# Performance work log

Hardware: AMD Instinct MI355X
Metric: run time of the kernel (lower is better)

## Reference

```python
import jax, jax.numpy as jnp
import numpy as np

N_NODES = 50000
N_EDGES = 800000
D = 128


def setup_inputs() -> dict:
    key = jax.random.key(0)
    k1, k2, k3, k4 = jax.random.split(key, 4)
    feat = jax.random.normal(k1, (N_NODES, D), dtype=jnp.float32)
    W = jax.random.normal(k2, (D, D), dtype=jnp.float32) * (1.0 / np.sqrt(D))
    b = jnp.zeros((D,), dtype=jnp.float32)
    eps = jnp.zeros((1,), dtype=jnp.float32)
    src = jax.random.randint(k3, (N_EDGES,), 0, N_NODES, dtype=jnp.int64 if jax.config.jax_enable_x64 else jnp.int32)
    dst = jax.random.randint(k4, (N_EDGES,), 0, N_NODES, dtype=jnp.int64 if jax.config.jax_enable_x64 else jnp.int32)
    return {"feat": feat, "W": W, "b": b, "eps": eps, "src": src, "dst": dst}


def reference(feat, W, b, eps, src, dst):
    # message passing: m_e = feat[src_e]; neigh_i = sum_{e: dst_e = i} m_e
    msgs = feat[src]  # [E, D] gather
    neigh = jax.ops.segment_sum(msgs, dst, num_segments=N_NODES)  # [N, D]
    # eps-weighted residual: (1 + eps) * h_dst + neigh
    rst = (1.0 + eps) * feat + neigh  # eps is [1], broadcasts
    # apply_func: Dense(D)
    out = jnp.einsum('nd,de->ne', rst, W) + b
    return out
```

## Files before the change

kernel.cpp:

```cpp
#include <hip/hip_runtime.h>

#define D 128
#define CAP 32
#define OCAP 4096
#define TILE 16

typedef __attribute__((ext_vector_type(8))) short bf16x8;
typedef __attribute__((ext_vector_type(4))) float f32x4;

static __device__ inline short f2bf(float f) {
  union { float f; unsigned u; } v; v.f = f;
  unsigned r = v.u + 0x7FFF + ((v.u >> 16) & 1);
  return (short)(r >> 16);
}
static __device__ inline float bf_lo(unsigned u) {
  union { unsigned u; float f; } v; v.u = u << 16; return v.f;
}
static __device__ inline float bf_hi(unsigned u) {
  union { unsigned u; float f; } v; v.u = u & 0xFFFF0000u; return v.f;
}

static __device__ inline void wfrag_build_one(const float* __restrict__ W,
                                              uint4* __restrict__ wfrag, int t) {
  int c = t >> 8, h = (t >> 6) & 3, l = t & 63;
  int col = c * 16 + (l & 15);
  int k0 = h * 32 + (l >> 4) * 8;
  unsigned u[4];
  #pragma unroll
  for (int p = 0; p < 4; ++p) {
    unsigned lo = (unsigned short)f2bf(W[(k0 + 2 * p) * D + col]);
    unsigned hi = (unsigned short)f2bf(W[(k0 + 2 * p + 1) * D + col]);
    u[p] = lo | (hi << 16);
  }
  wfrag[t] = make_uint4(u[0], u[1], u[2], u[3]);
}

__global__ __launch_bounds__(256) void build_kernel(
    const int* __restrict__ src, const int* __restrict__ dst,
    int* __restrict__ cnt, int* __restrict__ ocount, unsigned* __restrict__ oflow,
    unsigned short* __restrict__ permfix,
    const float* __restrict__ W, uint4* __restrict__ wfrag,
    const float* __restrict__ feat, uint4* __restrict__ featbf,
    int E, int ND8) {
  int grp = blockIdx.x & 7;
  int e = (blockIdx.x >> 3) * 256 + threadIdx.x;
  if (e < E) {
    int d = dst[e];
    if (((d >> 5) & 7) == grp) {
      int s = src[e];
      int c = atomicAdd(&cnt[d], 1);
      if (c < CAP) {
        permfix[(size_t)d * CAP + c] = (unsigned short)s;
      } else {
        int o = atomicAdd(ocount, 1);
        if (o < OCAP) oflow[o] = ((unsigned)d << 16) | (unsigned)s;
      }
    }
  }
  int i = blockIdx.x * 256 + threadIdx.x;
  if (i < ND8) {
    float4 u = ((const float4*)feat)[2 * i];
    float4 v = ((const float4*)feat)[2 * i + 1];
    unsigned w0 = (unsigned short)f2bf(u.x) | ((unsigned)(unsigned short)f2bf(u.y) << 16);
    unsigned w1 = (unsigned short)f2bf(u.z) | ((unsigned)(unsigned short)f2bf(u.w) << 16);
    unsigned w2 = (unsigned short)f2bf(v.x) | ((unsigned)(unsigned short)f2bf(v.y) << 16);
    unsigned w3 = (unsigned short)f2bf(v.z) | ((unsigned)(unsigned short)f2bf(v.w) << 16);
    featbf[i] = make_uint4(w0, w1, w2, w3);
  }
  if (i < 2048) wfrag_build_one(W, wfrag, i);
}

static __device__ inline void gather8m(uint4 q, int jb, int deg, int nm1,
                                       const uint2* __restrict__ featbf, int lane,
                                       float4& acc) {
  unsigned wds[4] = {q.x, q.y, q.z, q.w};
  uint2 r[8];
  #pragma unroll
  for (int k = 0; k < 4; ++k) {
    int s0 = (int)(wds[k] & 0xFFFFu);
    int s1 = (int)(wds[k] >> 16);
    s0 = min(s0, nm1);
    s1 = min(s1, nm1);
    r[2 * k]     = featbf[(size_t)s0 * 32 + lane];
    r[2 * k + 1] = featbf[(size_t)s1 * 32 + lane];
  }
  #pragma unroll
  for (int k = 0; k < 8; ++k) {
    bool v = (jb + k) < deg;
    unsigned x = v ? r[k].x : 0u;
    unsigned y = v ? r[k].y : 0u;
    acc.x += bf_lo(x); acc.y += bf_hi(x);
    acc.z += bf_lo(y); acc.w += bf_hi(y);
  }
}

__global__ __launch_bounds__(128, 4) void fused_gather_gemm(
    const uint2* __restrict__ featbf, const float* __restrict__ eps,
    const float* __restrict__ bias, const int* __restrict__ cnt,
    const int* __restrict__ ocount, const unsigned* __restrict__ oflow,
    const unsigned short* __restrict__ permfix,
    const uint4* __restrict__ wfrag, float* __restrict__ out, int N) {
  __shared__ float xs[TILE][132];
  __shared__ float sbias[128];
  int tid = threadIdx.x;
  int base = blockIdx.x * TILE;
  sbias[tid] = bias[tid];
  float scale = 1.0f + eps[0];
  int nm1 = N - 1;

  int g = tid >> 5, lane = tid & 31;
  #pragma unroll
  for (int it = 0; it < TILE / 4; ++it) {
    int lr = it * 4 + g;
    int grow = base + lr;
    float4 acc = make_float4(0.f, 0.f, 0.f, 0.f);
    if (grow < N) {
      const uint4* pf4 = (const uint4*)(permfix + (size_t)grow * CAP);
      int deg = cnt[grow];
      deg = (deg < CAP) ? deg : CAP;
      uint2 a0 = featbf[(size_t)grow * 32 + lane];
      uint4 q0 = pf4[0];
      uint4 q1 = pf4[1];
      acc.x = scale * bf_lo(a0.x);
      acc.y = scale * bf_hi(a0.x);
      acc.z = scale * bf_lo(a0.y);
      acc.w = scale * bf_hi(a0.y);
      gather8m(q0, 0, deg, nm1, featbf, lane, acc);
      gather8m(q1, 8, deg, nm1, featbf, lane, acc);
      if (deg > 16) {
        uint4 q2 = pf4[2];
        gather8m(q2, 16, deg, nm1, featbf, lane, acc);
        if (deg > 24) {
          uint4 q3 = pf4[3];
          gather8m(q3, 24, deg, nm1, featbf, lane, acc);
        }
      }
    }
    *(float4*)&xs[lr][lane * 4] = acc;
  }
  __syncthreads();

  int novf = *ocount;
  novf = (novf < OCAP) ? novf : OCAP;
  if (novf > 0) {
    if (tid < 32) {
      for (int o = 0; o < novf; ++o) {
        unsigned e = oflow[o];
        int d = (int)(e >> 16);
        if ((d / TILE) == (int)blockIdx.x) {
          int s = (int)(e & 0xFFFF);
          uint2 a = featbf[(size_t)s * 32 + tid];
          int r = d % TILE;
          xs[r][tid * 4 + 0] += bf_lo(a.x);
          xs[r][tid * 4 + 1] += bf_hi(a.x);
          xs[r][tid * 4 + 2] += bf_lo(a.y);
          xs[r][tid * 4 + 3] += bf_hi(a.y);
        }
      }
    }
    __syncthreads();
  }

  int w = tid >> 6;
  int l = tid & 63;
  int rowg = l >> 4, rl = l & 15;
  int cb = w * 4;

  bf16x8 a[4];
  #pragma unroll
  for (int h = 0; h < 4; ++h) {
    const float* p = &xs[rl][h * 32 + rowg * 8];
    float4 u = *(const float4*)p;
    float4 v = *(const float4*)(p + 4);
    bf16x8 t;
    t[0] = f2bf(u.x); t[1] = f2bf(u.y); t[2] = f2bf(u.z); t[3] = f2bf(u.w);
    t[4] = f2bf(v.x); t[5] = f2bf(v.y); t[6] = f2bf(v.z); t[7] = f2bf(v.w);
    a[h] = t;
  }

  const bf16x8* wf = (const bf16x8*)wfrag;
  #pragma unroll
  for (int cl = 0; cl < 4; ++cl) {
    int c = cb + cl;
    float bb = sbias[c * 16 + rl];
    f32x4 acc = {bb, bb, bb, bb};
    #pragma unroll
    for (int h = 0; h < 4; ++h) {
      bf16x8 b = wf[(c * 4 + h) * 64 + l];
      acc = __builtin_amdgcn_mfma_f32_16x16x32_bf16(a[h], b, acc, 0, 0, 0);
    }
    #pragma unroll
    for (int r = 0; r < 4; ++r) {
      int row = base + rowg * 4 + r;
      if (row < N) out[(size_t)row * D + c * 16 + rl] = acc[r];
    }
  }
}

__global__ __launch_bounds__(256) void init_out_kernel(
    const float* __restrict__ feat, const float* __restrict__ eps,
    float* __restrict__ out, int n4) {
  int i = blockIdx.x * blockDim.x + threadIdx.x;
  if (i >= n4) return;
  float scale = 1.0f + eps[0];
  float4 v = ((const float4*)feat)[i];
  v.x *= scale; v.y *= scale; v.z *= scale; v.w *= scale;
  ((float4*)out)[i] = v;
}

__global__ __launch_bounds__(256) void scatter_add_kernel(
    const float* __restrict__ feat, const int* __restrict__ src,
    const int* __restrict__ dst, float* __restrict__ out, int E) {
  int gid = blockIdx.x * blockDim.x + threadIdx.x;
  int e = gid >> 5;
  int lane = gid & 31;
  if (e >= E) return;
  int s = src[e], d = dst[e];
  float4 v = ((const float4*)(feat + (size_t)s * D))[lane];
  float* o = out + (size_t)d * D + lane * 4;
  unsafeAtomicAdd(o + 0, v.x);
  unsafeAtomicAdd(o + 1, v.y);
  unsafeAtomicAdd(o + 2, v.z);
  unsafeAtomicAdd(o + 3, v.w);
}

#define ROWS 64
__global__ __launch_bounds__(256) void gemm_inplace_kernel(
    float* __restrict__ out, const float* __restrict__ Wm,
    const float* __restrict__ bias, int N) {
  __shared__ float Ws[D * D];
  __shared__ float xs[ROWS * D];
  int tid = threadIdx.x;
  int base = blockIdx.x * ROWS;
  #pragma unroll
  for (int it = 0; it < 16; ++it) {
    int idx = tid + 256 * it;
    ((float4*)Ws)[idx] = ((const float4*)Wm)[idx];
  }
  #pragma unroll
  for (int it = 0; it < 8; ++it) {
    int idx = tid + 256 * it;
    int row = idx >> 5, c4 = idx & 31;
    float4 v = make_float4(0.f, 0.f, 0.f, 0.f);
    if (base + row < N) v = ((const float4*)(out + (size_t)(base + row) * D))[c4];
    ((float4*)xs)[row * 32 + c4] = v;
  }
  __syncthreads();
  int tc = tid & 31, tr = tid >> 5;
  float acc[8][4];
  #pragma unroll
  for (int r = 0; r < 8; ++r)
    #pragma unroll
    for (int i = 0; i < 4; ++i) acc[r][i] = 0.f;
  for (int k0 = 0; k0 < D; k0 += 4) {
    float4 f[8];
    #pragma unroll
    for (int r = 0; r < 8; ++r) f[r] = *(const float4*)&xs[(tr * 8 + r) * D + k0];
    float w[4][4];
    #pragma unroll
    for (int u = 0; u < 4; ++u)
      #pragma unroll
      for (int i = 0; i < 4; ++i) w[u][i] = Ws[(k0 + u) * D + tc + 32 * i];
    #pragma unroll
    for (int r = 0; r < 8; ++r)
      #pragma unroll
      for (int i = 0; i < 4; ++i) {
        acc[r][i] += f[r].x * w[0][i];
        acc[r][i] += f[r].y * w[1][i];
        acc[r][i] += f[r].z * w[2][i];
        acc[r][i] += f[r].w * w[3][i];
      }
  }
  float bv[4];
  #pragma unroll
  for (int i = 0; i < 4; ++i) bv[i] = bias[tc + 32 * i];
  #pragma unroll
  for (int r = 0; r < 8; ++r) {
    int row = base + tr * 8 + r;
    if (row < N) {
      #pragma unroll
      for (int i = 0; i < 4; ++i)
        out[(size_t)row * D + tc + 32 * i] = acc[r][i] + bv[i];
    }
  }
}

extern "C" void kernel_launch(void* const* d_in, const int* in_sizes, int n_in,
                              void* d_out, int out_size, void* d_ws, size_t ws_size,
                              hipStream_t stream) {
  const float* feat = (const float*)d_in[0];
  const float* Wm   = (const float*)d_in[1];
  const float* bias = (const float*)d_in[2];
  const float* eps  = (const float*)d_in[3];
  const int*   src  = (const int*)d_in[4];
  const int*   dst  = (const int*)d_in[5];
  float* out = (float*)d_out;

  int N = in_sizes[0] / D;
  int E = in_sizes[4];
  int ND8 = (N * D) / 8;

  size_t cnt_b    = (size_t)N * 4;
  size_t ocount_b = 4;
  size_t oflow_b  = (size_t)OCAP * 4;
  size_t perm_b   = (size_t)N * CAP * 2;
  size_t wfrag_off = (cnt_b + ocount_b + oflow_b + perm_b + 15) & ~(size_t)15;
  size_t featbf_off = wfrag_off + 2048 * 16;
  size_t needed = featbf_off + (size_t)N * D * 2;

  if (ws_size >= needed) {
    int* cnt = (int*)d_ws;
    int* ocount = cnt + N;
    unsigned* oflow = (unsigned*)(ocount + 1);
    unsigned short* permfix = (unsigned short*)(oflow + OCAP);
    uint4* wfrag = (uint4*)((char*)d_ws + wfrag_off);
    uint4* featbf = (uint4*)((char*)d_ws + featbf_off);

    hipMemsetAsync(cnt, 0, cnt_b + ocount_b, stream);

    int chunks = (E + 255) / 256;
    build_kernel<<<8 * chunks, 256, 0, stream>>>(
        src, dst, cnt, ocount, oflow, permfix, Wm, wfrag, feat, featbf, E, ND8);

    fused_gather_gemm<<<(N + TILE - 1) / TILE, 128, 0, stream>>>(
        (const uint2*)featbf, eps, bias, cnt, ocount, oflow, permfix, wfrag, out, N);
  } else {
    int n4 = (N * D) / 4;
    init_out_kernel<<<(n4 + 255) / 256, 256, 0, stream>>>(feat, eps, out, n4);
    long long total_threads = (long long)E * 32;
    int sblocks = (int)((total_threads + 255) / 256);
    scatter_add_kernel<<<sblocks, 256, 0, stream>>>(feat, src, dst, out, E);
    int gblocks2 = (N + ROWS - 1) / ROWS;
    gemm_inplace_kernel<<<gblocks2, 256, 0, stream>>>(out, Wm, bias, N);
  }
}
```

Before: 93.68 us.

## Split fused gather-GEMM into column-quarter gather kernel plus separate MFMA GEMM

Replaces the single fused gather+GEMM kernel with two kernels when the workspace is large enough. The first gathers neighbour features per node in column quarters, using more blocks and 8 lanes per node, and writes the bf16 residual sum to a workspace buffer. The second runs a bf16 MFMA GEMM over that buffer with bias. The aim is more parallelism and occupancy in the latency-bound gather, at the cost of an extra N×D bf16 round trip through memory, one more launch, and the overflow list being scanned four times as often.

```diff
diff --git a/kernel.cpp b/kernel.cpp
--- a/kernel.cpp
+++ b/kernel.cpp
@@ -12,6 +12,9 @@
   union { float f; unsigned u; } v; v.f = f;
   unsigned r = v.u + 0x7FFF + ((v.u >> 16) & 1);
   return (short)(r >> 16);
+}
+static __device__ inline unsigned pack2bf(float a, float b) {
+  return (unsigned)(unsigned short)f2bf(a) | ((unsigned)(unsigned short)f2bf(b) << 16);
 }
 static __device__ inline float bf_lo(unsigned u) {
   union { unsigned u; float f; } v; v.u = u << 16; return v.f;
@@ -27,11 +30,8 @@
   int k0 = h * 32 + (l >> 4) * 8;
   unsigned u[4];
   #pragma unroll
-  for (int p = 0; p < 4; ++p) {
-    unsigned lo = (unsigned short)f2bf(W[(k0 + 2 * p) * D + col]);
-    unsigned hi = (unsigned short)f2bf(W[(k0 + 2 * p + 1) * D + col]);
-    u[p] = lo | (hi << 16);
-  }
+  for (int p = 0; p < 4; ++p)
+    u[p] = pack2bf(W[(k0 + 2 * p) * D + col], W[(k0 + 2 * p + 1) * D + col]);
   wfrag[t] = make_uint4(u[0], u[1], u[2], u[3]);
 }
 
@@ -61,13 +61,122 @@
   if (i < ND8) {
     float4 u = ((const float4*)feat)[2 * i];
     float4 v = ((const float4*)feat)[2 * i + 1];
-    unsigned w0 = (unsigned short)f2bf(u.x) | ((unsigned)(unsigned short)f2bf(u.y) << 16);
-    unsigned w1 = (unsigned short)f2bf(u.z) | ((unsigned)(unsigned short)f2bf(u.w) << 16);
-    unsigned w2 = (unsigned short)f2bf(v.x) | ((unsigned)(unsigned short)f2bf(v.y) << 16);
-    unsigned w3 = (unsigned short)f2bf(v.z) | ((unsigned)(unsigned short)f2bf(v.w) << 16);
-    featbf[i] = make_uint4(w0, w1, w2, w3);
+    featbf[i] = make_uint4(pack2bf(u.x, u.y), pack2bf(u.z, u.w),
+                           pack2bf(v.x, v.y), pack2bf(v.z, v.w));
   }
   if (i < 2048) wfrag_build_one(W, wfrag, i);
+}
+
+static __device__ inline void gather8q(uint4 q, int jb, int deg, int nm1,
+                                       const uint2* __restrict__ featbf, int qoff,
+                                       float4& acc) {
+  unsigned wds[4] = {q.x, q.y, q.z, q.w};
+  uint2 r[8];
+  #pragma unroll
+  for (int k = 0; k < 4; ++k) {
+    int s0 = min((int)(wds[k] & 0xFFFFu), nm1);
+    int s1 = min((int)(wds[k] >> 16), nm1);
+    r[2 * k]     = featbf[(size_t)s0 * 32 + qoff];
+    r[2 * k + 1] = featbf[(size_t)s1 * 32 + qoff];
+  }
+  #pragma unroll
+  for (int k = 0; k < 8; ++k) {
+    bool v = (jb + k) < deg;
+    unsigned x = v ? r[k].x : 0u;
+    unsigned y = v ? r[k].y : 0u;
+    acc.x += bf_lo(x); acc.y += bf_hi(x);
+    acc.z += bf_lo(y); acc.w += bf_hi(y);
+  }
+}
+
+__global__ __launch_bounds__(128, 8) void gather_q_kernel(
+    const uint2* __restrict__ featbf, const float* __restrict__ eps,
+    const int* __restrict__ cnt, const int* __restrict__ ocount,
+    const unsigned* __restrict__ oflow, const unsigned short* __restrict__ permfix,
+    uint2* __restrict__ rst, int N, int ntiles) {
+  int j = blockIdx.x & 7;
+  int tile = (blockIdx.x >> 3) * 2 + (j >> 2);
+  if (tile >= ntiles) return;
+  int q = j & 3;
+  int tid = threadIdx.x;
+  int grp = tid >> 3;
+  int lane = tid & 7;
+  int node = tile * TILE + grp;
+  if (node >= N) return;
+  int qoff = q * 8 + lane;
+  float scale = 1.0f + eps[0];
+  int nm1 = N - 1;
+
+  uint2 a0 = featbf[(size_t)node * 32 + qoff];
+  float4 acc;
+  acc.x = scale * bf_lo(a0.x);
+  acc.y = scale * bf_hi(a0.x);
+  acc.z = scale * bf_lo(a0.y);
+  acc.w = scale * bf_hi(a0.y);
+
+  int deg = cnt[node];
+  deg = (deg < CAP) ? deg : CAP;
+  const uint4* pf4 = (const uint4*)(permfix + (size_t)node * CAP);
+  uint4 q0 = pf4[0];
+  uint4 q1 = pf4[1];
+  gather8q(q0, 0, deg, nm1, featbf, qoff, acc);
+  gather8q(q1, 8, deg, nm1, featbf, qoff, acc);
+  if (deg > 16) {
+    uint4 q2 = pf4[2];
+    gather8q(q2, 16, deg, nm1, featbf, qoff, acc);
+    if (deg > 24) {
+      uint4 q3 = pf4[3];
+      gather8q(q3, 24, deg, nm1, featbf, qoff, acc);
+    }
+  }
+  int novf = *ocount;
+  novf = (novf < OCAP) ? novf : OCAP;
+  for (int o = 0; o < novf; ++o) {
+    unsigned e = oflow[o];
+    if ((int)(e >> 16) == node) {
+      uint2 a = featbf[(size_t)(e & 0xFFFFu) * 32 + qoff];
+      acc.x += bf_lo(a.x); acc.y += bf_hi(a.x);
+      acc.z += bf_lo(a.y); acc.w += bf_hi(a.y);
+    }
+  }
+  rst[(size_t)node * 32 + qoff] = make_uint2(pack2bf(acc.x, acc.y), pack2bf(acc.z, acc.w));
+}
+
+__global__ __launch_bounds__(256, 8) void gemm_rst_kernel(
+    const bf16x8* __restrict__ rst, const float* __restrict__ bias,
+    const uint4* __restrict__ wfrag, float* __restrict__ out, int N) {
+  __shared__ float sbias[128];
+  int tid = threadIdx.x;
+  if (tid < 128) sbias[tid] = bias[tid];
+  __syncthreads();
+  int base = blockIdx.x * 64;
+  int w = tid >> 6;
+  int l = tid & 63;
+  int rowg = l >> 4, rl = l & 15;
+
+  int arow = base + 16 * w + rl;
+  int asafe = (arow < N) ? arow : (N - 1);
+  bf16x8 a[4];
+  #pragma unroll
+  for (int h = 0; h < 4; ++h)
+    a[h] = rst[(size_t)asafe * 16 + h * 4 + rowg];
+
+  const bf16x8* wf = (const bf16x8*)wfrag;
+  #pragma unroll
+  for (int c = 0; c < 8; ++c) {
+    float bb = sbias[c * 16 + rl];
+    f32x4 acc = {bb, bb, bb, bb};
+    #pragma unroll
+    for (int h = 0; h < 4; ++h) {
+      bf16x8 b = wf[(c * 4 + h) * 64 + l];
+      acc = __builtin_amdgcn_mfma_f32_16x16x32_bf16(a[h], b, acc, 0, 0, 0);
+    }
+    #pragma unroll
+    for (int r = 0; r < 4; ++r) {
+      int row = base + 16 * w + rowg * 4 + r;
+      if (row < N) out[(size_t)row * D + c * 16 + rl] = acc[r];
+    }
+  }
 }
 
 static __device__ inline void gather8m(uint4 q, int jb, int deg, int nm1,
@@ -77,10 +186,8 @@
   uint2 r[8];
   #pragma unroll
   for (int k = 0; k < 4; ++k) {
-    int s0 = (int)(wds[k] & 0xFFFFu);
-    int s1 = (int)(wds[k] >> 16);
-    s0 = min(s0, nm1);
-    s1 = min(s1, nm1);
+    int s0 = min((int)(wds[k] & 0xFFFFu), nm1);
+    int s1 = min((int)(wds[k] >> 16), nm1);
     r[2 * k]     = featbf[(size_t)s0 * 32 + lane];
     r[2 * k + 1] = featbf[(size_t)s1 * 32 + lane];
   }
@@ -306,9 +413,11 @@
   size_t perm_b   = (size_t)N * CAP * 2;
   size_t wfrag_off = (cnt_b + ocount_b + oflow_b + perm_b + 15) & ~(size_t)15;
   size_t featbf_off = wfrag_off + 2048 * 16;
-  size_t needed = featbf_off + (size_t)N * D * 2;
-
-  if (ws_size >= needed) {
+  size_t rst_off = featbf_off + (size_t)N * D * 2;
+  size_t needed_fused = rst_off;
+  size_t needed_full = rst_off + (size_t)N * D * 2;
+
+  if (ws_size >= needed_fused) {
     int* cnt = (int*)d_ws;
     int* ocount = cnt + N;
     unsigned* oflow = (unsigned*)(ocount + 1);
@@ -322,8 +431,18 @@
     build_kernel<<<8 * chunks, 256, 0, stream>>>(
         src, dst, cnt, ocount, oflow, permfix, Wm, wfrag, feat, featbf, E, ND8);
 
-    fused_gather_gemm<<<(N + TILE - 1) / TILE, 128, 0, stream>>>(
-        (const uint2*)featbf, eps, bias, cnt, ocount, oflow, permfix, wfrag, out, N);
+    int ntiles = (N + TILE - 1) / TILE;
+    if (ws_size >= needed_full) {
+      uint2* rst = (uint2*)((char*)d_ws + rst_off);
+      int supers = (ntiles + 1) / 2;
+      gather_q_kernel<<<supers * 8, 128, 0, stream>>>(
+          (const uint2*)featbf, eps, cnt, ocount, oflow, permfix, rst, N, ntiles);
+      gemm_rst_kernel<<<(N + 63) / 64, 256, 0, stream>>>(
+          (const bf16x8*)rst, bias, wfrag, out, N);
+    } else {
+      fused_gather_gemm<<<ntiles, 128, 0, stream>>>(
+          (const uint2*)featbf, eps, bias, cnt, ocount, oflow, permfix, wfrag, out, N);
+    }
   } else {
     int n4 = (N * D) / 4;
     init_out_kernel<<<(n4 + 255) / 256, 256, 0, stream>>>(feat, eps, out, n4);
```

New measurement: 137.5 us. 46.7% more time.
